# Performance work log

Hardware: AMD Instinct MI355X
Metric: run time of the kernel (lower is better)

Reference implementation:

```python
import jax, jax.numpy as jnp
import numpy as np

# DeformConv3d hyperparams (from init_kwargs)
STRIDE = (1, 1, 1)
PAD = (1, 1, 1)
DIL = (1, 1, 1)
GROUPS = 1
DEFORM_GROUPS = 1  # reference assumes dg == 1


def setup_inputs() -> dict:
    key = jax.random.key(0)
    k1, k2, k3, k4 = jax.random.split(key, 4)
    x = jax.random.normal(k1, (2, 32, 24, 24, 24), jnp.float32)
    # offset channels = 3 * dg * kD*kH*kW = 81, layout [k_idx, (dz,dy,dx)]
    offset = jax.random.normal(k2, (2, 81, 24, 24, 24), jnp.float32)
    weight = jax.random.normal(k3, (64, 32, 3, 3, 3), jnp.float32) * 0.05
    bias = jax.random.normal(k4, (64,), jnp.float32) * 0.05
    return {"x": x, "offset": offset, "weight": weight, "bias": bias}


def _deform_conv3d(x, offset, weight, bias):
    B, C, D, H, W = x.shape
    Cout, Cg, kD, kH, kW = weight.shape
    sD, sH, sW = STRIDE
    pD, pH, pW = PAD
    dD, dH, dW = DIL
    Kn = kD * kH * kW
    Do = (D + 2 * pD - dD * (kD - 1) - 1) // sD + 1
    Ho = (H + 2 * pH - dH * (kH - 1) - 1) // sH + 1
    Wo = (W + 2 * pW - dW * (kW - 1) - 1) // sW + 1
    N = Do * Ho * Wo

    # offset: [B, Kn*3, Do,Ho,Wo] -> [B, Kn, 3, N]
    off = offset.reshape(B, Kn, 3, N)

    # kernel tap grid [Kn]
    kz, ky, kx = jnp.meshgrid(jnp.arange(kD), jnp.arange(kH), jnp.arange(kW), indexing='ij')
    kz, ky, kx = kz.reshape(Kn), ky.reshape(Kn), kx.reshape(Kn)
    # output grid [N]
    oz, oy, ox = jnp.meshgrid(jnp.arange(Do), jnp.arange(Ho), jnp.arange(Wo), indexing='ij')
    oz, oy, ox = oz.reshape(N), oy.reshape(N), ox.reshape(N)

    # sampling coords [B, Kn, N]
    z = (oz[None, None, :] * sD - pD) + kz[None, :, None] * dD + off[:, :, 0]
    y = (oy[None, None, :] * sH - pH) + ky[None, :, None] * dH + off[:, :, 1]
    xx = (ox[None, None, :] * sW - pW) + kx[None, :, None] * dW + off[:, :, 2]

    z0 = jnp.floor(z); fz = z - z0
    y0 = jnp.floor(y); fy = y - y0
    x0 = jnp.floor(xx); fx = xx - x0

    x_flat = x.reshape(B, C, D * H * W)
    acc = jnp.zeros((B, C, Kn * N), x.dtype)
    # 8 trilinear corners (fixed small loop)
    for dz in (0, 1):
        iz = z0 + dz
        wz = fz if dz else (1.0 - fz)
        for dy in (0, 1):
            iy = y0 + dy
            wy = fy if dy else (1.0 - fy)
            for dx in (0, 1):
                ix = x0 + dx
                wx = fx if dx else (1.0 - fx)
                valid = ((iz >= 0) & (iz < D) & (iy >= 0) & (iy < H)
                         & (ix >= 0) & (ix < W))
                w = (wz * wy * wx) * valid.astype(x.dtype)  # [B,Kn,N]
                izc = jnp.clip(iz, 0, D - 1).astype(jnp.int32)
                iyc = jnp.clip(iy, 0, H - 1).astype(jnp.int32)
                ixc = jnp.clip(ix, 0, W - 1).astype(jnp.int32)
                idx = (izc * H + iyc) * W + ixc  # [B,Kn,N]
                g = jnp.take_along_axis(x_flat, idx.reshape(B, 1, Kn * N), axis=2)
                acc = acc + g * w.reshape(B, 1, Kn * N)

    # im2col columns ordered (c, kz, ky, kx) to match weight layout
    cols = acc.reshape(B, C * Kn, N)
    Cpg = C // GROUPS
    Opg = Cout // GROUPS
    cols_g = cols.reshape(B, GROUPS, Cpg * Kn, N)
    w_g = weight.reshape(GROUPS, Opg, Cpg * Kn)
    out = jnp.einsum('gok,bgkn->bgon', w_g, cols_g).reshape(B, Cout, N)
    out = out + bias[None, :, None]
    return out.reshape(B, Cout, Do, Ho, Wo)


def reference(x, offset, weight, bias):
    return _deform_conv3d(x, offset, weight, bias)
```

## Files before the change

kernel.cpp:

```cpp
#include <hip/hip_runtime.h>
#include <hip/hip_fp16.h>


constexpr int B   = 2;
constexpr int C   = 32;
constexpr int D   = 24, H = 24, W = 24;
constexpr int CO  = 64;
constexpr int KN  = 27;
constexpr int DHW = D * H * W;
constexpr int N   = DHW;
constexpr int CK  = C * KN;

constexpr int LD   = 10;
constexpr int MB   = 3;
constexpr int NVOX = LD * LD * LD;

constexpr int TPB_MAIN = 256;
constexpr int NBLK     = B * 6 * 6 * 6;

constexpr int PREPX_BLKS = (B * DHW) / 256;
constexpr int PREPW_BLKS = (CO * CK) / 256;

using h8v   = __attribute__((ext_vector_type(8))) _Float16;
using f32x4 = __attribute__((ext_vector_type(4))) float;

__device__ __forceinline__ h8v splat8(float w) {
    const _Float16 h = (_Float16)w;
    h8v r;
    #pragma unroll
    for (int i = 0; i < 8; ++i) r[i] = h;
    return r;
}

__device__ __forceinline__ unsigned pack2h(float a, float b) {
    const _Float16 ha = (_Float16)a, hb = (_Float16)b;
    unsigned short ua, ub;
    __builtin_memcpy(&ua, &ha, 2);
    __builtin_memcpy(&ub, &hb, 2);
    return (unsigned)ua | ((unsigned)ub << 16);
}

__global__ __launch_bounds__(256)
void prep_fused(const float* __restrict__ x, const float* __restrict__ wgt,
                _Float16* __restrict__ xT, _Float16* __restrict__ wp) {
    const int bid = blockIdx.x;
    if (bid < PREPX_BLKS) {
        __shared__ unsigned s_t[256 * 21];
        const int tid = threadIdx.x;
        const int v0  = bid * 256;
        const int b   = (v0 >= DHW) ? 1 : 0;
        const int vox = (v0 - b * DHW) + tid;
        const float* xb = x + (size_t)(b * C) * DHW + vox;
        #pragma unroll
        for (int c2 = 0; c2 < 16; ++c2) {
            const float f0 = xb[(size_t)(2 * c2)     * DHW];
            const float f1 = xb[(size_t)(2 * c2 + 1) * DHW];
            s_t[tid * 21 + c2] = pack2h(f0, f1);
        }
        __syncthreads();
        unsigned r[16];
        #pragma unroll
        for (int j = 0; j < 16; ++j) r[j] = s_t[tid * 21 + j];
        int4* dst = reinterpret_cast<int4*>(xT + ((size_t)(v0 + tid)) * 32);
        dst[0] = make_int4(r[0],  r[1],  r[2],  r[3]);
        dst[1] = make_int4(r[4],  r[5],  r[6],  r[7]);
        dst[2] = make_int4(r[8],  r[9],  r[10], r[11]);
        dst[3] = make_int4(r[12], r[13], r[14], r[15]);
    } else {
        const int idx   = (bid - PREPX_BLKS) * 256 + threadIdx.x;
        const int j     = idx & 7;
        const int lane  = (idx >> 3) & 63;
        const int t     = idx >> 9;
        const int otile = t / 27;
        const int kstep = t - otile * 27;
        const int o     = otile * 16 + (lane & 15);
        const int c     = 8 * (lane >> 4) + j;
        wp[idx] = (_Float16)wgt[(size_t)o * CK + c * KN + kstep];
    }
}

__device__ __forceinline__ int clamp0(int v, int hi) {
    return min(max(v, 0), hi);
}

__global__ __launch_bounds__(TPB_MAIN)
void deform_main(const float* __restrict__ off,
                 const _Float16* __restrict__ xT,
                 const _Float16* __restrict__ wp,
                 const float* __restrict__ bias,
                 float* __restrict__ out) {
    __shared__ h8v s_x[NVOX * 4];

    const int tid  = threadIdx.x;
    const int lane = tid & 63;
    const int wv   = tid >> 6;
    const int p    = lane & 15;
    const int q    = lane >> 4;

    int t = blockIdx.x;
    int b = 0;
    if (t >= 216) { b = 1; t -= 216; }
    const int tz = t / 36;
    const int rt = t - tz * 36;
    const int ty = rt / 6;
    const int tx = rt - ty * 6;
    const int oz0 = tz * 4, oy0 = ty * 4, ox0 = tx * 4;
    const int tbz = oz0 - MB, tby = oy0 - MB, tbx = ox0 - MB;

    const h8v* xbase = reinterpret_cast<const h8v*>(xT) + (size_t)b * DHW * 4;

    for (int i = tid; i < NVOX * 4; i += TPB_MAIN) {
        const int v  = i >> 2;
        const int c  = i & 3;
        const int vz = v / 100;
        const int vr = v - vz * 100;
        const int vy = vr / 10;
        const int vx = vr - vy * 10;
        const int gz = clamp0(tbz + vz, D - 1);
        const int gy = clamp0(tby + vy, H - 1);
        const int gx = clamp0(tbx + vx, W - 1);
        const int gvox = (gz * H + gy) * W + gx;
        s_x[v * 4 + ((c + v) & 3)] = xbase[(size_t)gvox * 4 + c];
    }
    __syncthreads();

    const int pz = wv, py = p >> 2, px = p & 3;
    const int oz = oz0 + pz, oy = oy0 + py, ox = ox0 + px;
    const int n  = (oz * H + oy) * W + ox;
    const float* offp  = off + (size_t)(b * 81) * N + n;
    const h8v*   wbase = reinterpret_cast<const h8v*>(wp);

    f32x4 acc[4];
    #pragma unroll
    for (int ot = 0; ot < 4; ++ot) acc[ot] = (f32x4){0.f, 0.f, 0.f, 0.f};

    #pragma unroll 1
    for (int ks = 0; ks < KN; ++ks) {
        const int kz = ks / 9;
        const int kr = ks - kz * 9;
        const int ky = kr / 3;
        const int kx = kr - ky * 3;

        const float offz = offp[(size_t)(ks * 3 + 0) * N];
        const float offy = offp[(size_t)(ks * 3 + 1) * N];
        const float offx = offp[(size_t)(ks * 3 + 2) * N];

        h8v afr[4];
        #pragma unroll
        for (int ot = 0; ot < 4; ++ot)
            afr[ot] = wbase[(ot * 27 + ks) * 64 + lane];

        const float z  = (float)(oz - 1 + kz) + offz;
        const float y  = (float)(oy - 1 + ky) + offy;
        const float xx = (float)(ox - 1 + kx) + offx;
        const float zf = floorf(z), yf = floorf(y), xf = floorf(xx);
        const float fz = z - zf, fy = y - yf, fx = xx - xf;
        const int z0 = (int)zf, y0 = (int)yf, x0 = (int)xf;

        float cw[8];
        #pragma unroll
        for (int cr = 0; cr < 8; ++cr) {
            const int cz = cr >> 2, cy = (cr >> 1) & 1, cx = cr & 1;
            const int iz = z0 + cz, iy = y0 + cy, ix = x0 + cx;
            const bool vd = ((unsigned)iz < (unsigned)D) &&
                            ((unsigned)iy < (unsigned)H) &&
                            ((unsigned)ix < (unsigned)W);
            const float wz = cz ? fz : 1.0f - fz;
            const float wy = cy ? fy : 1.0f - fy;
            const float wx = cx ? fx : 1.0f - fx;
            cw[cr] = vd ? (wz * wy * wx) : 0.0f;
        }

        const int rz = z0 - tbz, ry = y0 - tby, rx = x0 - tbx;
        const bool in = ((unsigned)rz < (unsigned)(LD - 1)) &&
                        ((unsigned)ry < (unsigned)(LD - 1)) &&
                        ((unsigned)rx < (unsigned)(LD - 1));

        h8v v8[8];
        if (in) {
            const int rv0 = (rz * LD + ry) * LD + rx;
            #pragma unroll
            for (int cr = 0; cr < 8; ++cr) {
                const int rv = rv0 + (cr >> 2) * 100 + ((cr >> 1) & 1) * 10
                             + (cr & 1);
                v8[cr] = s_x[rv * 4 + ((q + rv) & 3)];
            }
        }
        if (!in) {
            #pragma unroll
            for (int cr = 0; cr < 8; ++cr) {
                const int cz = cr >> 2, cy = (cr >> 1) & 1, cx = cr & 1;
                const int izc = clamp0(z0 + cz, D - 1);
                const int iyc = clamp0(y0 + cy, H - 1);
                const int ixc = clamp0(x0 + cx, W - 1);
                const int gvox = (izc * H + iyc) * W + ixc;
                v8[cr] = xbase[(size_t)gvox * 4 + q];
            }
        }

        h8v bfr = splat8(0.0f);
        #pragma unroll
        for (int cr = 0; cr < 8; ++cr)
            bfr += v8[cr] * splat8(cw[cr]);

        #pragma unroll
        for (int ot = 0; ot < 4; ++ot)
            acc[ot] = __builtin_amdgcn_mfma_f32_16x16x32_f16(afr[ot], bfr,
                                                             acc[ot], 0, 0, 0);
    }

    #pragma unroll
    for (int ot = 0; ot < 4; ++ot) {
        #pragma unroll
        for (int r = 0; r < 4; ++r) {
            const int o = ot * 16 + q * 4 + r;
            out[((size_t)(b * CO + o)) * N + n] = acc[ot][r] + bias[o];
        }
    }
}

extern "C" void kernel_launch(void* const* d_in, const int* in_sizes, int n_in,
                              void* d_out, int out_size, void* d_ws, size_t ws_size,
                              hipStream_t stream) {
    const float* x    = (const float*)d_in[0];
    const float* off  = (const float*)d_in[1];
    const float* wgt  = (const float*)d_in[2];
    const float* bias = (const float*)d_in[3];
    float* out = (float*)d_out;

    _Float16* xT = (_Float16*)d_ws;
    _Float16* wp = (_Float16*)((char*)d_ws + 1769472);

    prep_fused<<<PREPX_BLKS + PREPW_BLKS, 256, 0, stream>>>(x, wgt, xT, wp);
    deform_main<<<NBLK, TPB_MAIN, 0, stream>>>(off, xT, wp, bias, out);
}
```

Baseline: 104.7 us.

## Split kernel taps across wave pairs, halve z-tile, add block swizzle and offset prefetch

Output tiles shrink to 2x4x4, which doubles the block count to 864. Each pair of waves now handles one z-slice and splits the 27 kernel taps between its two waves, with a shared-memory reduction before the store. The change also software-prefetches the next tap's offsets, permutes the block index to spread tiles across XCDs, and sets launch_bounds occupancy to 3. The aim is more parallelism, better latency hiding and better occupancy. In exchange it adds an extra sync and reduction, and the halo tile overlap is larger relative to the useful work.

```diff
diff --git a/kernel.cpp b/kernel.cpp
--- a/kernel.cpp
+++ b/kernel.cpp
@@ -11,12 +11,13 @@
 constexpr int N   = DHW;
 constexpr int CK  = C * KN;
 
-constexpr int LD   = 10;
-constexpr int MB   = 3;
-constexpr int NVOX = LD * LD * LD;
+constexpr int TZ = 2, TY = 4, TX = 4;
+constexpr int LDZ = 8, LDY = 10, LDX = 10;
+constexpr int NVOX = LDZ * LDY * LDX;
+constexpr int MBM  = 3;
 
 constexpr int TPB_MAIN = 256;
-constexpr int NBLK     = B * 6 * 6 * 6;
+constexpr int NBLK     = B * 12 * 6 * 6;
 
 constexpr int PREPX_BLKS = (B * DHW) / 256;
 constexpr int PREPW_BLKS = (CO * CK) / 256;
@@ -83,7 +84,7 @@
     return min(max(v, 0), hi);
 }
 
-__global__ __launch_bounds__(TPB_MAIN)
+__global__ __launch_bounds__(TPB_MAIN, 3)
 void deform_main(const float* __restrict__ off,
                  const _Float16* __restrict__ xT,
                  const _Float16* __restrict__ wp,
@@ -94,28 +95,31 @@
     const int tid  = threadIdx.x;
     const int lane = tid & 63;
     const int wv   = tid >> 6;
+    const int pg   = wv >> 1;
+    const int kh   = wv & 1;
     const int p    = lane & 15;
     const int q    = lane >> 4;
 
-    int t = blockIdx.x;
+    const int bid = blockIdx.x;
+    int t = (bid & 7) * 108 + (bid >> 3);
     int b = 0;
-    if (t >= 216) { b = 1; t -= 216; }
+    if (t >= 432) { b = 1; t -= 432; }
     const int tz = t / 36;
     const int rt = t - tz * 36;
     const int ty = rt / 6;
     const int tx = rt - ty * 6;
-    const int oz0 = tz * 4, oy0 = ty * 4, ox0 = tx * 4;
-    const int tbz = oz0 - MB, tby = oy0 - MB, tbx = ox0 - MB;
+    const int oz0 = tz * TZ, oy0 = ty * TY, ox0 = tx * TX;
+    const int tbz = oz0 - MBM, tby = oy0 - MBM, tbx = ox0 - MBM;
 
     const h8v* xbase = reinterpret_cast<const h8v*>(xT) + (size_t)b * DHW * 4;
 
     for (int i = tid; i < NVOX * 4; i += TPB_MAIN) {
         const int v  = i >> 2;
         const int c  = i & 3;
-        const int vz = v / 100;
-        const int vr = v - vz * 100;
-        const int vy = vr / 10;
-        const int vx = vr - vy * 10;
+        const int vz = v / (LDY * LDX);
+        const int vr = v - vz * (LDY * LDX);
+        const int vy = vr / LDX;
+        const int vx = vr - vy * LDX;
         const int gz = clamp0(tbz + vz, D - 1);
         const int gy = clamp0(tby + vy, H - 1);
         const int gx = clamp0(tbx + vx, W - 1);
@@ -124,26 +128,34 @@
     }
     __syncthreads();
 
-    const int pz = wv, py = p >> 2, px = p & 3;
+    const int pz = pg, py = p >> 2, px = p & 3;
     const int oz = oz0 + pz, oy = oy0 + py, ox = ox0 + px;
     const int n  = (oz * H + oy) * W + ox;
     const float* offp  = off + (size_t)(b * 81) * N + n;
     const h8v*   wbase = reinterpret_cast<const h8v*>(wp);
 
+    const int k0 = kh ? 14 : 0;
+    const int k1 = kh ? 27 : 14;
+
     f32x4 acc[4];
     #pragma unroll
     for (int ot = 0; ot < 4; ++ot) acc[ot] = (f32x4){0.f, 0.f, 0.f, 0.f};
 
+    float offz = offp[(size_t)(k0 * 3 + 0) * N];
+    float offy = offp[(size_t)(k0 * 3 + 1) * N];
+    float offx = offp[(size_t)(k0 * 3 + 2) * N];
+
     #pragma unroll 1
-    for (int ks = 0; ks < KN; ++ks) {
+    for (int ks = k0; ks < k1; ++ks) {
+        const int kn = (ks + 1 < k1) ? (ks + 1) : ks;
+        const float nfz = offp[(size_t)(kn * 3 + 0) * N];
+        const float nfy = offp[(size_t)(kn * 3 + 1) * N];
+        const float nfx = offp[(size_t)(kn * 3 + 2) * N];
+
         const int kz = ks / 9;
         const int kr = ks - kz * 9;
         const int ky = kr / 3;
         const int kx = kr - ky * 3;
-
-        const float offz = offp[(size_t)(ks * 3 + 0) * N];
-        const float offy = offp[(size_t)(ks * 3 + 1) * N];
-        const float offx = offp[(size_t)(ks * 3 + 2) * N];
 
         h8v afr[4];
         #pragma unroll
@@ -172,17 +184,17 @@
         }
 
         const int rz = z0 - tbz, ry = y0 - tby, rx = x0 - tbx;
-        const bool in = ((unsigned)rz < (unsigned)(LD - 1)) &&
-                        ((unsigned)ry < (unsigned)(LD - 1)) &&
-                        ((unsigned)rx < (unsigned)(LD - 1));
+        const bool in = ((unsigned)rz < (unsigned)(LDZ - 1)) &&
+                        ((unsigned)ry < (unsigned)(LDY - 1)) &&
+                        ((unsigned)rx < (unsigned)(LDX - 1));
 
         h8v v8[8];
         if (in) {
-            const int rv0 = (rz * LD + ry) * LD + rx;
+            const int rv0 = (rz * LDY + ry) * LDX + rx;
             #pragma unroll
             for (int cr = 0; cr < 8; ++cr) {
-                const int rv = rv0 + (cr >> 2) * 100 + ((cr >> 1) & 1) * 10
-                             + (cr & 1);
+                const int rv = rv0 + (cr >> 2) * (LDY * LDX)
+                             + ((cr >> 1) & 1) * LDX + (cr & 1);
                 v8[cr] = s_x[rv * 4 + ((q + rv) & 3)];
             }
         }
@@ -207,14 +219,34 @@
         for (int ot = 0; ot < 4; ++ot)
             acc[ot] = __builtin_amdgcn_mfma_f32_16x16x32_f16(afr[ot], bfr,
                                                              acc[ot], 0, 0, 0);
-    }
-
-    #pragma unroll
-    for (int ot = 0; ot < 4; ++ot) {
-        #pragma unroll
-        for (int r = 0; r < 4; ++r) {
-            const int o = ot * 16 + q * 4 + r;
-            out[((size_t)(b * CO + o)) * N + n] = acc[ot][r] + bias[o];
+
+        offz = nfz; offy = nfy; offx = nfx;
+    }
+
+    __syncthreads();
+    float4* s_red = reinterpret_cast<float4*>(s_x);
+    if (kh == 1) {
+        float4* dst = &s_red[((size_t)pg * 64 + lane) * 4];
+        #pragma unroll
+        for (int ot = 0; ot < 4; ++ot)
+            dst[ot] = make_float4(acc[ot][0], acc[ot][1], acc[ot][2], acc[ot][3]);
+    }
+    __syncthreads();
+    if (kh == 0) {
+        const float4* src = &s_red[((size_t)pg * 64 + lane) * 4];
+        #pragma unroll
+        for (int ot = 0; ot < 4; ++ot) {
+            const float4 tv = src[ot];
+            acc[ot][0] += tv.x; acc[ot][1] += tv.y;
+            acc[ot][2] += tv.z; acc[ot][3] += tv.w;
+        }
+        #pragma unroll
+        for (int ot = 0; ot < 4; ++ot) {
+            #pragma unroll
+            for (int r = 0; r < 4; ++r) {
+                const int o = ot * 16 + q * 4 + r;
+                out[((size_t)(b * CO + o)) * N + n] = acc[ot][r] + bias[o];
+            }
         }
     }
 }
```

Result: faster. 100.7 us (-3.8%).
